# Kernel optimization log

Measured on AMD Instinct MI355X. Metric: run time of the kernel, lower is better.

## Reference

```python
import jax, jax.numpy as jnp
import numpy as np

N_HEADS = 16


def setup_inputs() -> dict:
    key = jax.random.key(0)
    ks = jax.random.split(key, 8)
    B, S, D = 4, 2048, 1024
    scale = 1.0 / np.sqrt(D)
    return {
        "x": jax.random.normal(ks[0], (B, S, D), dtype=jnp.float32),
        "Wq": jax.random.normal(ks[1], (D, D), dtype=jnp.float32) * scale,
        "bq": jax.random.normal(ks[2], (D,), dtype=jnp.float32) * 0.01,
        "Wk": jax.random.normal(ks[3], (D, D), dtype=jnp.float32) * scale,
        "bk": jax.random.normal(ks[4], (D,), dtype=jnp.float32) * 0.01,
        "Wv": jax.random.normal(ks[5], (D, D), dtype=jnp.float32) * scale,
        "bv": jax.random.normal(ks[6], (D,), dtype=jnp.float32) * 0.01,
        "mask": jax.random.randint(ks[7], (B, S), 0, 2, dtype=jnp.int32),
    }


def reference(x, Wq, bq, Wk, bk, Wv, bv, mask):
    B, S, D = x.shape
    H = N_HEADS
    W = D // H
    # QKV projections (Linear with weight stored input-major: y = x @ W + b)
    q = (x @ Wq + bq).reshape(B, S, H, W).transpose(0, 2, 1, 3)  # (B,H,S,W)
    k = (x @ Wk + bk).reshape(B, S, H, W).transpose(0, 2, 1, 3)
    v = (x @ Wv + bv).reshape(B, S, H, W).transpose(0, 2, 1, 3)
    # scaled dot-product scores: (B,H,S,S)
    scores = jnp.einsum("bhsw,bhtw->bhst", q, k) / jnp.sqrt(jnp.asarray(W, x.dtype))
    # mask==1 means masked (subtract large constant), per original code
    scores = scores - 10000.0 * mask[:, None, None, :].astype(x.dtype)
    attn = jax.nn.softmax(scores, axis=-1)  # dropout p=0 -> identity
    h = jnp.einsum("bhst,bhtw->bhsw", attn, v)  # (B,H,S,W)
    h = h.transpose(0, 2, 1, 3).reshape(B, S, D)
    return h
```

## Files before the change

kernel.cpp:

```cpp
#include <hip/hip_runtime.h>
#include <math.h>

#define B_NUM 4
#define S_LEN 2048
#define D_DIM 1024
#define H_NUM 16
#define W_DIM 64

typedef float4 f4;
typedef _Float16 f16;
typedef f16 f16x8 __attribute__((ext_vector_type(8)));
typedef f16 f16x4 __attribute__((ext_vector_type(4)));
typedef float floatx4 __attribute__((ext_vector_type(4)));

#define GLOAD_LDS16(gp, lp)                                                     \
    __builtin_amdgcn_global_load_lds(                                           \
        (const __attribute__((address_space(1))) void*)(gp),                    \
        (__attribute__((address_space(3))) void*)(lp), 16, 0, 0)

__global__ __launch_bounds__(256) void compact_kernel(
    const int* __restrict__ mask, short* __restrict__ fwdmap,
    int* __restrict__ cnt)
{
    __shared__ int sc[256];
    const int b   = blockIdx.x;
    const int tid = threadIdx.x;
    const int t0  = tid * 8;

#pragma unroll
    for (int j = 0; j < 8; ++j) fwdmap[b * S_LEN + t0 + j] = 0;

    int kept[8], c = 0;
#pragma unroll
    for (int j = 0; j < 8; ++j) {
        kept[j] = (mask[b * S_LEN + t0 + j] == 0);
        c += kept[j];
    }
    sc[tid] = c;
    __syncthreads();
    for (int off = 1; off < 256; off <<= 1) {
        int add = (tid >= off) ? sc[tid - off] : 0;
        __syncthreads();
        sc[tid] += add;
        __syncthreads();
    }
    int base = sc[tid] - c;
#pragma unroll
    for (int j = 0; j < 8; ++j)
        if (kept[j]) fwdmap[b * S_LEN + (base++)] = (short)(t0 + j);
    if (tid == 255) {
        cnt[b * 4 + 0] = sc[255];
        cnt[b * 4 + 1] = (sc[255] + 63) & ~63;
        cnt[b * 4 + 2] = (sc[255] + 127) & ~127;
    }
}

__global__ __launch_bounds__(256) void cast_x_kernel(
    const float* __restrict__ x, f16* __restrict__ x16)
{
    const size_t i = (size_t)blockIdx.x * 256 + threadIdx.x;
    f4 t = *(const f4*)&x[i * 4];
    f16x4 o;
    o[0] = (f16)t.x; o[1] = (f16)t.y; o[2] = (f16)t.z; o[3] = (f16)t.w;
    *(f16x4*)&x16[i * 4] = o;
}

__global__ __launch_bounds__(256) void transpose_w_kernel(
    const float* __restrict__ Wq, const float* __restrict__ Wk,
    const float* __restrict__ Wv, f16* __restrict__ wt16)
{
    __shared__ float ts[64][68];

    const int tid = threadIdx.x;
    const int k0 = blockIdx.x * 64;
    const int n0 = blockIdx.y * 64;
    const float* Wsel = (blockIdx.z == 0) ? Wq : (blockIdx.z == 1) ? Wk : Wv;
    f16* outp = wt16 + (size_t)blockIdx.z * D_DIM * D_DIM;

    const int r  = tid >> 4;
    const int c4 = (tid & 15) * 4;
#pragma unroll
    for (int i = 0; i < 4; ++i) {
        f4 t = *(const f4*)&Wsel[(size_t)(k0 + r + i * 16) * D_DIM + n0 + c4];
        *(f4*)&ts[r + i * 16][c4] = t;
    }
    __syncthreads();
#pragma unroll
    for (int i = 0; i < 4; ++i) {
        int idx = tid + i * 256;
        int nl = idx >> 4;
        int k4 = (idx & 15) * 4;
        f16x4 o;
#pragma unroll
        for (int j = 0; j < 4; ++j) o[j] = (f16)ts[k4 + j][nl];
        *(f16x4*)&outp[(size_t)(n0 + nl) * D_DIM + k0 + k4] = o;
    }
}

__global__ __launch_bounds__(256) void qkv_mfma_kernel(
    const f16* __restrict__ x16, const f16* __restrict__ wt16,
    const float* __restrict__ bq, const float* __restrict__ bk,
    const float* __restrict__ bv, const short* __restrict__ fwdmap,
    const int* __restrict__ cnt,
    f16* __restrict__ Qo, f16* __restrict__ Ko, f16* __restrict__ Vo)
{
    __shared__ f16 As[128 * 64];
    __shared__ f16 Bs[128 * 64];

    const int tid  = threadIdx.x;
    const int lane = tid & 63;
    const int wid  = tid >> 6;
    const int lx   = lane & 15;
    const int quad = lane >> 4;
    const int wm   = wid >> 1;
    const int wn   = wid & 1;

    const int r0    = blockIdx.y * 128;
    const int nt    = blockIdx.x;
    const int midx  = nt >> 3;
    const int c0    = (nt & 7) * 128;
    const int bB    = r0 >> 11;
    const int r0loc = r0 & (S_LEN - 1);

    if (midx > 0 && r0loc >= cnt[bB * 4 + 2]) return;

    const f16* Bg = wt16 + (size_t)midx * D_DIM * D_DIM + (size_t)c0 * D_DIM;

    const int srow = lane >> 3;
    const int scw  = ((lane & 7) ^ srow) * 8;

    int arows[4];
#pragma unroll
    for (int it = 0; it < 4; ++it) {
        int rl = (wid * 4 + it) * 8 + srow;
        arows[it] = (midx == 0)
            ? (r0 + rl)
            : (bB * S_LEN + (int)fwdmap[bB * S_LEN + r0loc + rl]);
    }

    floatx4 acc[4][4];
#pragma unroll
    for (int a = 0; a < 4; ++a)
#pragma unroll
        for (int b = 0; b < 4; ++b) { acc[a][b][0]=0.f; acc[a][b][1]=0.f; acc[a][b][2]=0.f; acc[a][b][3]=0.f; }

    for (int k0 = 0; k0 < D_DIM; k0 += 64) {
        __syncthreads();
#pragma unroll
        for (int it = 0; it < 4; ++it) {
            int chunk = wid * 4 + it;
            GLOAD_LDS16(&x16[(size_t)arows[it] * D_DIM + k0 + scw], &As[chunk * 512]);
            GLOAD_LDS16(&Bg[(size_t)(chunk * 8 + srow) * D_DIM + k0 + scw], &Bs[chunk * 512]);
        }
        __syncthreads();

#pragma unroll
        for (int kh = 0; kh < 2; ++kh) {
            const int csw = ((kh * 4 + quad) ^ (lx & 7)) * 8;
            f16x8 af[4], bf[4];
#pragma unroll
            for (int tm = 0; tm < 4; ++tm)
                af[tm] = *(const f16x8*)&As[(wm * 64 + tm * 16 + lx) * 64 + csw];
#pragma unroll
            for (int tn = 0; tn < 4; ++tn)
                bf[tn] = *(const f16x8*)&Bs[(wn * 64 + tn * 16 + lx) * 64 + csw];
#pragma unroll
            for (int tm = 0; tm < 4; ++tm)
#pragma unroll
                for (int tn = 0; tn < 4; ++tn)
                    acc[tm][tn] = __builtin_amdgcn_mfma_f32_16x16x32_f16(
                        af[tm], bf[tn], acc[tm][tn], 0, 0, 0);
        }
    }

    const float* bp = (midx == 0) ? bq : (midx == 1) ? bk : bv;
    float bias[4];
#pragma unroll
    for (int tn = 0; tn < 4; ++tn)
        bias[tn] = bp[c0 + wn * 64 + tn * 16 + lx];

    if (midx == 0) {
#pragma unroll
        for (int tm = 0; tm < 4; ++tm) {
            int s = r0loc + wm * 64 + tm * 16 + quad * 4;
#pragma unroll
            for (int tn = 0; tn < 4; ++tn) {
                int gc = c0 + wn * 64 + tn * 16 + lx;
                int h = gc >> 6, w = gc & 63;
                size_t base = (((size_t)(bB * H_NUM + h)) * S_LEN + s) * W_DIM + w;
#pragma unroll
                for (int rr = 0; rr < 4; ++rr)
                    Qo[base + (size_t)rr * W_DIM] =
                        (f16)((acc[tm][tn][rr] + bias[tn]) * 0.125f);
            }
        }
    } else if (midx == 1) {
#pragma unroll
        for (int tm = 0; tm < 4; ++tm) {
            int jc = r0loc + wm * 64 + tm * 16 + quad * 4;
#pragma unroll
            for (int tn = 0; tn < 4; ++tn) {
                int gc = c0 + wn * 64 + tn * 16 + lx;
                int h = gc >> 6, w = gc & 63;
                size_t base = (((size_t)(bB * H_NUM + h)) * S_LEN + jc) * W_DIM + w;
#pragma unroll
                for (int rr = 0; rr < 4; ++rr)
                    Ko[base + (size_t)rr * W_DIM] = (f16)(acc[tm][tn][rr] + bias[tn]);
            }
        }
    } else {
#pragma unroll
        for (int tm = 0; tm < 4; ++tm) {
            int jc = r0loc + wm * 64 + tm * 16 + quad * 4;
#pragma unroll
            for (int tn = 0; tn < 4; ++tn) {
                int gc = c0 + wn * 64 + tn * 16 + lx;
                int h = gc >> 6, w = gc & 63;
                f16x4 v;
#pragma unroll
                for (int rr = 0; rr < 4; ++rr) v[rr] = (f16)(acc[tm][tn][rr] + bias[tn]);
                *(f16x4*)&Vo[(((size_t)(bB * H_NUM + h)) * W_DIM + w) * S_LEN + jc] = v;
            }
        }
    }
}

#define LSTR 72

__global__ __launch_bounds__(256) void attn_kernel(
    const f16* __restrict__ Q, const f16* __restrict__ Kc,
    const f16* __restrict__ Vct, const int* __restrict__ cnt,
    float* __restrict__ out)
{
    __shared__ f16 Ks[64][LSTR];
    __shared__ f16 Vs[64][LSTR];

    const int tid  = threadIdx.x;
    const int lane = tid & 63;
    const int wid  = tid >> 6;
    const int lx   = lane & 15;
    const int quad = lane >> 4;
    const int qt = blockIdx.x, h = blockIdx.y, bb = blockIdx.z;

    const int count = cnt[bb * 4 + 0];
    const int scp   = cnt[bb * 4 + 1];

    const size_t hoff = ((size_t)(bb * H_NUM + h)) * S_LEN * W_DIM;
    const f16* Qg = Q + hoff + (size_t)qt * 128 * W_DIM;
    const f16* Kg = Kc + hoff;
    const f16* Vg = Vct + hoff;

    f16x8 qb[2][2];
#pragma unroll
    for (int u = 0; u < 2; ++u) {
        int qrow = u * 64 + wid * 16 + lx;
        qb[u][0] = *(const f16x8*)&Qg[(size_t)qrow * W_DIM + quad * 8];
        qb[u][1] = *(const f16x8*)&Qg[(size_t)qrow * W_DIM + 32 + quad * 8];
    }

    floatx4 o[2][4];
    float lsum[2] = {0.f, 0.f};
#pragma unroll
    for (int u = 0; u < 2; ++u)
#pragma unroll
        for (int wb = 0; wb < 4; ++wb) { o[u][wb][0]=0.f; o[u][wb][1]=0.f; o[u][wb][2]=0.f; o[u][wb][3]=0.f; }

    for (int k0 = 0; k0 < scp; k0 += 64) {
        __syncthreads();
#pragma unroll
        for (int it = 0; it < 2; ++it) {
            int idx = tid + it * 256;
            int row = idx >> 3, c8 = (idx & 7) * 8;
            *(f16x8*)&Ks[row][c8] = *(const f16x8*)&Kg[(size_t)(k0 + row) * W_DIM + c8];
            *(f16x8*)&Vs[row][c8] = *(const f16x8*)&Vg[(size_t)row * S_LEN + k0 + c8];
        }
        __syncthreads();

        const bool tail = (k0 + 64 > count);

        f16x4 pb[2][4];
#pragma unroll
        for (int n = 0; n < 4; ++n) {
            f16x8 ka0 = *(const f16x8*)&Ks[n * 16 + lx][quad * 8];
            f16x8 ka1 = *(const f16x8*)&Ks[n * 16 + lx][32 + quad * 8];
            const int kb = k0 + n * 16 + quad * 4;
#pragma unroll
            for (int u = 0; u < 2; ++u) {
                floatx4 s; s[0]=0.f; s[1]=0.f; s[2]=0.f; s[3]=0.f;
                s = __builtin_amdgcn_mfma_f32_16x16x32_f16(ka0, qb[u][0], s, 0, 0, 0);
                s = __builtin_amdgcn_mfma_f32_16x16x32_f16(ka1, qb[u][1], s, 0, 0, 0);
                float p[4], ls = 0.f;
                if (tail) {
#pragma unroll
                    for (int r = 0; r < 4; ++r) {
                        float sv = (kb + r < count) ? s[r] : -1.0e4f;
                        p[r] = __expf(sv); ls += p[r];
                    }
                } else {
#pragma unroll
                    for (int r = 0; r < 4; ++r) { p[r] = __expf(s[r]); ls += p[r]; }
                }
                lsum[u] += ls;
#pragma unroll
                for (int r = 0; r < 4; ++r) pb[u][n][r] = (f16)p[r];
            }
        }

#pragma unroll
        for (int wb = 0; wb < 4; ++wb) {
#pragma unroll
            for (int n = 0; n < 4; ++n) {
                f16x4 va = *(const f16x4*)&Vs[wb * 16 + lx][n * 16 + quad * 4];
#pragma unroll
                for (int u = 0; u < 2; ++u)
                    o[u][wb] = __builtin_amdgcn_mfma_f32_16x16x16f16(va, pb[u][n], o[u][wb], 0, 0, 0);
            }
        }
    }

#pragma unroll
    for (int u = 0; u < 2; ++u) {
        float ls = lsum[u];
        ls += __shfl_xor(ls, 16);
        ls += __shfl_xor(ls, 32);
        const float rl = 1.0f / ls;
        const int q = qt * 128 + u * 64 + wid * 16 + lx;
        const size_t base = ((size_t)bb * S_LEN + q) * D_DIM + h * W_DIM;
#pragma unroll
        for (int wb = 0; wb < 4; ++wb) {
            f4 r;
            r.x = o[u][wb][0] * rl;
            r.y = o[u][wb][1] * rl;
            r.z = o[u][wb][2] * rl;
            r.w = o[u][wb][3] * rl;
            *(f4*)&out[base + wb * 16 + quad * 4] = r;
        }
    }
}

extern "C" void kernel_launch(void* const* d_in, const int* in_sizes, int n_in,
                              void* d_out, int out_size, void* d_ws, size_t ws_size,
                              hipStream_t stream)
{
    const float* x    = (const float*)d_in[0];
    const float* Wq   = (const float*)d_in[1];
    const float* bq   = (const float*)d_in[2];
    const float* Wk   = (const float*)d_in[3];
    const float* bk   = (const float*)d_in[4];
    const float* Wv   = (const float*)d_in[5];
    const float* bv   = (const float*)d_in[6];
    const int*   mask = (const int*)d_in[7];
    float* out = (float*)d_out;

    const size_t per = (size_t)B_NUM * H_NUM * S_LEN * W_DIM;
    f16*   Q      = (f16*)d_ws;
    f16*   Kc     = Q + per;
    f16*   Vct    = Kc + per;
    f16*   x16    = Vct + per;
    f16*   wt16   = x16 + (size_t)(B_NUM * S_LEN) * D_DIM;
    int*   cnt    = (int*)(wt16 + (size_t)3 * D_DIM * D_DIM);
    short* fwdmap = (short*)(cnt + 4 * B_NUM);

    compact_kernel<<<B_NUM, 256, 0, stream>>>(mask, fwdmap, cnt);
    cast_x_kernel<<<(B_NUM * S_LEN * D_DIM) / 1024, 256, 0, stream>>>(x, x16);
    transpose_w_kernel<<<dim3(16, 16, 3), 256, 0, stream>>>(Wq, Wk, Wv, wt16);
    qkv_mfma_kernel<<<dim3(24, 64), 256, 0, stream>>>(
        x16, wt16, bq, bk, bv, fwdmap, cnt, Q, Kc, Vct);
    attn_kernel<<<dim3(S_LEN / 128, H_NUM, B_NUM), 256, 0, stream>>>(
        Q, Kc, Vct, cnt, out);
}
```

Baseline: 222.2 us.

## Merge prep kernels into one launch and make QKV GEMM persistent with atomic tile queue

The mask compaction, x cast and weight transpose kernels are folded into a single prep kernel that dispatches by block index, replacing three launches with one. The QKV GEMM becomes a persistent kernel of 1280 blocks that pull tiles from an atomic ticket counter. Tiles skipped by the mask-based early exit no longer leave empty block slots, which evens out load across CUs. The costs are an atomic plus two barriers per tile, and the ticket must be reset by the prep kernel on every call.

Result: slower. 227.1 us (+2.2%).

```diff
diff --git a/kernel.cpp b/kernel.cpp
--- a/kernel.cpp
+++ b/kernel.cpp
@@ -18,82 +18,84 @@
         (const __attribute__((address_space(1))) void*)(gp),                    \
         (__attribute__((address_space(3))) void*)(lp), 16, 0, 0)
 
-__global__ __launch_bounds__(256) void compact_kernel(
-    const int* __restrict__ mask, short* __restrict__ fwdmap,
-    int* __restrict__ cnt)
-{
-    __shared__ int sc[256];
-    const int b   = blockIdx.x;
-    const int tid = threadIdx.x;
-    const int t0  = tid * 8;
-
-#pragma unroll
-    for (int j = 0; j < 8; ++j) fwdmap[b * S_LEN + t0 + j] = 0;
-
-    int kept[8], c = 0;
-#pragma unroll
-    for (int j = 0; j < 8; ++j) {
-        kept[j] = (mask[b * S_LEN + t0 + j] == 0);
-        c += kept[j];
-    }
-    sc[tid] = c;
-    __syncthreads();
-    for (int off = 1; off < 256; off <<= 1) {
-        int add = (tid >= off) ? sc[tid - off] : 0;
-        __syncthreads();
-        sc[tid] += add;
-        __syncthreads();
-    }
-    int base = sc[tid] - c;
-#pragma unroll
-    for (int j = 0; j < 8; ++j)
-        if (kept[j]) fwdmap[b * S_LEN + (base++)] = (short)(t0 + j);
-    if (tid == 255) {
-        cnt[b * 4 + 0] = sc[255];
-        cnt[b * 4 + 1] = (sc[255] + 63) & ~63;
-        cnt[b * 4 + 2] = (sc[255] + 127) & ~127;
-    }
-}
-
-__global__ __launch_bounds__(256) void cast_x_kernel(
-    const float* __restrict__ x, f16* __restrict__ x16)
-{
-    const size_t i = (size_t)blockIdx.x * 256 + threadIdx.x;
-    f4 t = *(const f4*)&x[i * 4];
-    f16x4 o;
-    o[0] = (f16)t.x; o[1] = (f16)t.y; o[2] = (f16)t.z; o[3] = (f16)t.w;
-    *(f16x4*)&x16[i * 4] = o;
-}
-
-__global__ __launch_bounds__(256) void transpose_w_kernel(
+#define N_TILES 1536
+#define GEMM_BLOCKS 1280
+
+__global__ __launch_bounds__(256) void prep_kernel(
+    const float* __restrict__ x,
     const float* __restrict__ Wq, const float* __restrict__ Wk,
-    const float* __restrict__ Wv, f16* __restrict__ wt16)
+    const float* __restrict__ Wv, const int* __restrict__ mask,
+    f16* __restrict__ x16, f16* __restrict__ wt16,
+    short* __restrict__ fwdmap, int* __restrict__ cnt, int* __restrict__ ticket)
 {
     __shared__ float ts[64][68];
-
+    const int bid = blockIdx.x;
     const int tid = threadIdx.x;
-    const int k0 = blockIdx.x * 64;
-    const int n0 = blockIdx.y * 64;
-    const float* Wsel = (blockIdx.z == 0) ? Wq : (blockIdx.z == 1) ? Wk : Wv;
-    f16* outp = wt16 + (size_t)blockIdx.z * D_DIM * D_DIM;
-
-    const int r  = tid >> 4;
-    const int c4 = (tid & 15) * 4;
-#pragma unroll
-    for (int i = 0; i < 4; ++i) {
-        f4 t = *(const f4*)&Wsel[(size_t)(k0 + r + i * 16) * D_DIM + n0 + c4];
-        *(f4*)&ts[r + i * 16][c4] = t;
-    }
-    __syncthreads();
-#pragma unroll
-    for (int i = 0; i < 4; ++i) {
-        int idx = tid + i * 256;
-        int nl = idx >> 4;
-        int k4 = (idx & 15) * 4;
+
+    if (bid < 4) {
+        int* sc = (int*)&ts[0][0];
+        const int b  = bid;
+        const int t0 = tid * 8;
+        if (bid == 0 && tid == 0) *ticket = 0;
+
+#pragma unroll
+        for (int j = 0; j < 8; ++j) fwdmap[b * S_LEN + t0 + j] = 0;
+
+        int kept[8], c = 0;
+#pragma unroll
+        for (int j = 0; j < 8; ++j) {
+            kept[j] = (mask[b * S_LEN + t0 + j] == 0);
+            c += kept[j];
+        }
+        sc[tid] = c;
+        __syncthreads();
+        for (int off = 1; off < 256; off <<= 1) {
+            int add = (tid >= off) ? sc[tid - off] : 0;
+            __syncthreads();
+            sc[tid] += add;
+            __syncthreads();
+        }
+        int base = sc[tid] - c;
+#pragma unroll
+        for (int j = 0; j < 8; ++j)
+            if (kept[j]) fwdmap[b * S_LEN + (base++)] = (short)(t0 + j);
+        if (tid == 255) {
+            cnt[b * 4 + 0] = sc[255];
+            cnt[b * 4 + 1] = (sc[255] + 63) & ~63;
+            cnt[b * 4 + 2] = (sc[255] + 127) & ~127;
+        }
+    } else if (bid < 4 + 768) {
+        const int tb = bid - 4;
+        const int k0 = (tb & 15) * 64;
+        const int n0 = ((tb >> 4) & 15) * 64;
+        const int z  = tb >> 8;
+        const float* Wsel = (z == 0) ? Wq : (z == 1) ? Wk : Wv;
+        f16* outp = wt16 + (size_t)z * D_DIM * D_DIM;
+
+        const int r  = tid >> 4;
+        const int c4 = (tid & 15) * 4;
+#pragma unroll
+        for (int i = 0; i < 4; ++i) {
+            f4 t = *(const f4*)&Wsel[(size_t)(k0 + r + i * 16) * D_DIM + n0 + c4];
+            *(f4*)&ts[r + i * 16][c4] = t;
+        }
+        __syncthreads();
+#pragma unroll
+        for (int i = 0; i < 4; ++i) {
+            int idx = tid + i * 256;
+            int nl = idx >> 4;
+            int k4 = (idx & 15) * 4;
+            f16x4 o;
+#pragma unroll
+            for (int j = 0; j < 4; ++j) o[j] = (f16)ts[k4 + j][nl];
+            *(f16x4*)&outp[(size_t)(n0 + nl) * D_DIM + k0 + k4] = o;
+        }
+    } else {
+        const size_t i = (size_t)(bid - 772) * 256 + tid;
+        f4 t = *(const f4*)&x[i * 4];
         f16x4 o;
-#pragma unroll
-        for (int j = 0; j < 4; ++j) o[j] = (f16)ts[k4 + j][nl];
-        *(f16x4*)&outp[(size_t)(n0 + nl) * D_DIM + k0 + k4] = o;
+        o[0] = (f16)t.x; o[1] = (f16)t.y; o[2] = (f16)t.z; o[3] = (f16)t.w;
+        *(f16x4*)&x16[i * 4] = o;
     }
 }
 
@@ -101,11 +103,12 @@
     const f16* __restrict__ x16, const f16* __restrict__ wt16,
     const float* __restrict__ bq, const float* __restrict__ bk,
     const float* __restrict__ bv, const short* __restrict__ fwdmap,
-    const int* __restrict__ cnt,
+    const int* __restrict__ cnt, int* __restrict__ ticket,
     f16* __restrict__ Qo, f16* __restrict__ Ko, f16* __restrict__ Vo)
 {
     __shared__ f16 As[128 * 64];
     __shared__ f16 Bs[128 * 64];
+    __shared__ int s_t;
 
     const int tid  = threadIdx.x;
     const int lane = tid & 63;
@@ -115,111 +118,120 @@
     const int wm   = wid >> 1;
     const int wn   = wid & 1;
 
-    const int r0    = blockIdx.y * 128;
-    const int nt    = blockIdx.x;
-    const int midx  = nt >> 3;
-    const int c0    = (nt & 7) * 128;
-    const int bB    = r0 >> 11;
-    const int r0loc = r0 & (S_LEN - 1);
-
-    if (midx > 0 && r0loc >= cnt[bB * 4 + 2]) return;
-
-    const f16* Bg = wt16 + (size_t)midx * D_DIM * D_DIM + (size_t)c0 * D_DIM;
-
     const int srow = lane >> 3;
     const int scw  = ((lane & 7) ^ srow) * 8;
 
-    int arows[4];
-#pragma unroll
-    for (int it = 0; it < 4; ++it) {
-        int rl = (wid * 4 + it) * 8 + srow;
-        arows[it] = (midx == 0)
-            ? (r0 + rl)
-            : (bB * S_LEN + (int)fwdmap[bB * S_LEN + r0loc + rl]);
-    }
-
-    floatx4 acc[4][4];
-#pragma unroll
-    for (int a = 0; a < 4; ++a)
-#pragma unroll
-        for (int b = 0; b < 4; ++b) { acc[a][b][0]=0.f; acc[a][b][1]=0.f; acc[a][b][2]=0.f; acc[a][b][3]=0.f; }
-
-    for (int k0 = 0; k0 < D_DIM; k0 += 64) {
-        __syncthreads();
+    for (;;) {
+        __syncthreads();
+        if (tid == 0) s_t = atomicAdd(ticket, 1);
+        __syncthreads();
+        const int t = s_t;
+        if (t >= N_TILES) return;
+
+        const int nt    = t % 24;
+        const int mt    = t / 24;
+        const int midx  = nt >> 3;
+        const int c0    = (nt & 7) * 128;
+        const int r0    = mt * 128;
+        const int bB    = r0 >> 11;
+        const int r0loc = r0 & (S_LEN - 1);
+
+        if (midx > 0 && r0loc >= cnt[bB * 4 + 2]) continue;
+
+        const f16* Bg = wt16 + (size_t)midx * D_DIM * D_DIM + (size_t)c0 * D_DIM;
+
+        int arows[4];
 #pragma unroll
         for (int it = 0; it < 4; ++it) {
-            int chunk = wid * 4 + it;
-            GLOAD_LDS16(&x16[(size_t)arows[it] * D_DIM + k0 + scw], &As[chunk * 512]);
-            GLOAD_LDS16(&Bg[(size_t)(chunk * 8 + srow) * D_DIM + k0 + scw], &Bs[chunk * 512]);
-        }
-        __syncthreads();
-
-#pragma unroll
-        for (int kh = 0; kh < 2; ++kh) {
-            const int csw = ((kh * 4 + quad) ^ (lx & 7)) * 8;
-            f16x8 af[4], bf[4];
-#pragma unroll
-            for (int tm = 0; tm < 4; ++tm)
-                af[tm] = *(const f16x8*)&As[(wm * 64 + tm * 16 + lx) * 64 + csw];
-#pragma unroll
-            for (int tn = 0; tn < 4; ++tn)
-                bf[tn] = *(const f16x8*)&Bs[(wn * 64 + tn * 16 + lx) * 64 + csw];
-#pragma unroll
-            for (int tm = 0; tm < 4; ++tm)
+            int rl = (wid * 4 + it) * 8 + srow;
+            arows[it] = (midx == 0)
+                ? (r0 + rl)
+                : (bB * S_LEN + (int)fwdmap[bB * S_LEN + r0loc + rl]);
+        }
+
+        floatx4 acc[4][4];
+#pragma unroll
+        for (int a = 0; a < 4; ++a)
+#pragma unroll
+            for (int b = 0; b < 4; ++b) { acc[a][b][0]=0.f; acc[a][b][1]=0.f; acc[a][b][2]=0.f; acc[a][b][3]=0.f; }
+
+        for (int k0 = 0; k0 < D_DIM; k0 += 64) {
+            __syncthreads();
+#pragma unroll
+            for (int it = 0; it < 4; ++it) {
+                int chunk = wid * 4 + it;
+                GLOAD_LDS16(&x16[(size_t)arows[it] * D_DIM + k0 + scw], &As[chunk * 512]);
+                GLOAD_LDS16(&Bg[(size_t)(chunk * 8 + srow) * D_DIM + k0 + scw], &Bs[chunk * 512]);
+            }
+            __syncthreads();
+
+#pragma unroll
+            for (int kh = 0; kh < 2; ++kh) {
+                const int csw = ((kh * 4 + quad) ^ (lx & 7)) * 8;
+                f16x8 af[4], bf[4];
+#pragma unroll
+                for (int tm = 0; tm < 4; ++tm)
+                    af[tm] = *(const f16x8*)&As[(wm * 64 + tm * 16 + lx) * 64 + csw];
 #pragma unroll
                 for (int tn = 0; tn < 4; ++tn)
-                    acc[tm][tn] = __builtin_amdgcn_mfma_f32_16x16x32_f16(
-                        af[tm], bf[tn], acc[tm][tn], 0, 0, 0);
-        }
-    }
-
-    const float* bp = (midx == 0) ? bq : (midx == 1) ? bk : bv;
-    float bias[4];
-#pragma unroll
-    for (int tn = 0; tn < 4; ++tn)
-        bias[tn] = bp[c0 + wn * 64 + tn * 16 + lx];
-
-    if (midx == 0) {
-#pragma unroll
-        for (int tm = 0; tm < 4; ++tm) {
-            int s = r0loc + wm * 64 + tm * 16 + quad * 4;
-#pragma unroll
-            for (int tn = 0; tn < 4; ++tn) {
-                int gc = c0 + wn * 64 + tn * 16 + lx;
-                int h = gc >> 6, w = gc & 63;
-                size_t base = (((size_t)(bB * H_NUM + h)) * S_LEN + s) * W_DIM + w;
-#pragma unroll
-                for (int rr = 0; rr < 4; ++rr)
-                    Qo[base + (size_t)rr * W_DIM] =
-                        (f16)((acc[tm][tn][rr] + bias[tn]) * 0.125f);
-            }
-        }
-    } else if (midx == 1) {
-#pragma unroll
-        for (int tm = 0; tm < 4; ++tm) {
-            int jc = r0loc + wm * 64 + tm * 16 + quad * 4;
-#pragma unroll
-            for (int tn = 0; tn < 4; ++tn) {
-                int gc = c0 + wn * 64 + tn * 16 + lx;
-                int h = gc >> 6, w = gc & 63;
-                size_t base = (((size_t)(bB * H_NUM + h)) * S_LEN + jc) * W_DIM + w;
-#pragma unroll
-                for (int rr = 0; rr < 4; ++rr)
-                    Ko[base + (size_t)rr * W_DIM] = (f16)(acc[tm][tn][rr] + bias[tn]);
-            }
-        }
-    } else {
-#pragma unroll
-        for (int tm = 0; tm < 4; ++tm) {
-            int jc = r0loc + wm * 64 + tm * 16 + quad * 4;
-#pragma unroll
-            for (int tn = 0; tn < 4; ++tn) {
-                int gc = c0 + wn * 64 + tn * 16 + lx;
-                int h = gc >> 6, w = gc & 63;
-                f16x4 v;
-#pragma unroll
-                for (int rr = 0; rr < 4; ++rr) v[rr] = (f16)(acc[tm][tn][rr] + bias[tn]);
-                *(f16x4*)&Vo[(((size_t)(bB * H_NUM + h)) * W_DIM + w) * S_LEN + jc] = v;
+                    bf[tn] = *(const f16x8*)&Bs[(wn * 64 + tn * 16 + lx) * 64 + csw];
+#pragma unroll
+                for (int tm = 0; tm < 4; ++tm)
+#pragma unroll
+                    for (int tn = 0; tn < 4; ++tn)
+                        acc[tm][tn] = __builtin_amdgcn_mfma_f32_16x16x32_f16(
+                            af[tm], bf[tn], acc[tm][tn], 0, 0, 0);
+            }
+        }
+
+        const float* bp = (midx == 0) ? bq : (midx == 1) ? bk : bv;
+        float bias[4];
+#pragma unroll
+        for (int tn = 0; tn < 4; ++tn)
+            bias[tn] = bp[c0 + wn * 64 + tn * 16 + lx];
+
+        if (midx == 0) {
+#pragma unroll
+            for (int tm = 0; tm < 4; ++tm) {
+                int s = r0loc + wm * 64 + tm * 16 + quad * 4;
+#pragma unroll
+                for (int tn = 0; tn < 4; ++tn) {
+                    int gc = c0 + wn * 64 + tn * 16 + lx;
+                    int h = gc >> 6, w = gc & 63;
+                    size_t base = (((size_t)(bB * H_NUM + h)) * S_LEN + s) * W_DIM + w;
+#pragma unroll
+                    for (int rr = 0; rr < 4; ++rr)
+                        Qo[base + (size_t)rr * W_DIM] =
+                            (f16)((acc[tm][tn][rr] + bias[tn]) * 0.125f);
+                }
+            }
+        } else if (midx == 1) {
+#pragma unroll
+            for (int tm = 0; tm < 4; ++tm) {
+                int jc = r0loc + wm * 64 + tm * 16 + quad * 4;
+#pragma unroll
+                for (int tn = 0; tn < 4; ++tn) {
+                    int gc = c0 + wn * 64 + tn * 16 + lx;
+                    int h = gc >> 6, w = gc & 63;
+                    size_t base = (((size_t)(bB * H_NUM + h)) * S_LEN + jc) * W_DIM + w;
+#pragma unroll
+                    for (int rr = 0; rr < 4; ++rr)
+                        Ko[base + (size_t)rr * W_DIM] = (f16)(acc[tm][tn][rr] + bias[tn]);
+                }
+            }
+        } else {
+#pragma unroll
+            for (int tm = 0; tm < 4; ++tm) {
+                int jc = r0loc + wm * 64 + tm * 16 + quad * 4;
+#pragma unroll
+                for (int tn = 0; tn < 4; ++tn) {
+                    int gc = c0 + wn * 64 + tn * 16 + lx;
+                    int h = gc >> 6, w = gc & 63;
+                    f16x4 v;
+#pragma unroll
+                    for (int rr = 0; rr < 4; ++rr) v[rr] = (f16)(acc[tm][tn][rr] + bias[tn]);
+                    *(f16x4*)&Vo[(((size_t)(bB * H_NUM + h)) * W_DIM + w) * S_LEN + jc] = v;
+                }
             }
         }
     }
@@ -359,13 +371,13 @@
     f16*   x16    = Vct + per;
     f16*   wt16   = x16 + (size_t)(B_NUM * S_LEN) * D_DIM;
     int*   cnt    = (int*)(wt16 + (size_t)3 * D_DIM * D_DIM);
-    short* fwdmap = (short*)(cnt + 4 * B_NUM);
-
-    compact_kernel<<<B_NUM, 256, 0, stream>>>(mask, fwdmap, cnt);
-    cast_x_kernel<<<(B_NUM * S_LEN * D_DIM) / 1024, 256, 0, stream>>>(x, x16);
-    transpose_w_kernel<<<dim3(16, 16, 3), 256, 0, stream>>>(Wq, Wk, Wv, wt16);
-    qkv_mfma_kernel<<<dim3(24, 64), 256, 0, stream>>>(
-        x16, wt16, bq, bk, bv, fwdmap, cnt, Q, Kc, Vct);
+    int*   ticket = cnt + 4 * B_NUM;
+    short* fwdmap = (short*)(ticket + 4);
+
+    prep_kernel<<<4 + 768 + 8192, 256, 0, stream>>>(
+        x, Wq, Wk, Wv, mask, x16, wt16, fwdmap, cnt, ticket);
+    qkv_mfma_kernel<<<GEMM_BLOCKS, 256, 0, stream>>>(
+        x16, wt16, bq, bk, bv, fwdmap, cnt, ticket, Q, Kc, Vct);
     attn_kernel<<<dim3(S_LEN / 128, H_NUM, B_NUM), 256, 0, stream>>>(
         Q, Kc, Vct, cnt, out);
 }
```
